# Kernel optimization log

Measured on AMD Instinct MI355X. Metric: run time of the kernel, lower is better.

## Reference

```python
import jax, jax.numpy as jnp
import numpy as np

B, C, H, W = 4, 256, 64, 64
CQ = C // 4


def setup_inputs() -> dict:
    key = jax.random.key(0)
    ks = jax.random.split(key, 16)
    s = 0.05
    return {
        "x1": jax.random.normal(ks[0], (B, C, H, W), jnp.float32),
        "x2": jax.random.normal(ks[1], (B, C, H, W), jnp.float32),
        "x3": jax.random.normal(ks[2], (B, C, H, W), jnp.float32),
        "xt": jax.random.normal(ks[3], (B, C, H, W), jnp.float32),
        "Wq": jax.random.normal(ks[4], (CQ, C), jnp.float32) * s,
        "bq": jax.random.normal(ks[5], (CQ,), jnp.float32) * s,
        "Wk": jax.random.normal(ks[6], (CQ, C), jnp.float32) * s,
        "bk": jax.random.normal(ks[7], (CQ,), jnp.float32) * s,
        "Wk2": jax.random.normal(ks[8], (CQ, C), jnp.float32) * s,
        "bk2": jax.random.normal(ks[9], (CQ,), jnp.float32) * s,
        "Wv": jax.random.normal(ks[10], (C, C), jnp.float32) * s,
        "bv": jax.random.normal(ks[11], (C,), jnp.float32) * s,
        "Wv2": jax.random.normal(ks[12], (C, C), jnp.float32) * s,
        "bv2": jax.random.normal(ks[13], (C,), jnp.float32) * s,
        "gamma": jax.random.normal(ks[14], (1,), jnp.float32) * 0.1,
        "gamma2": jax.random.normal(ks[15], (1,), jnp.float32) * 0.1,
    }


def _conv1x1(Wt, b, x):
    # 1x1 conv == per-pixel linear: (O, C) x (B, C, H, W) -> (B, O, H, W)
    return jnp.einsum('oc,bchw->bohw', Wt, x) + b[None, :, None, None]


def reference(x1, x2, x3, xt, Wq, bq, Wk, bk, Wk2, bk2, Wv, bv, Wv2, bv2, gamma, gamma2):
    b_, c_, h_, w_ = x1.shape
    n = h_ * w_
    q = _conv1x1(Wq, bq, x3).reshape(b_, -1, n)      # (B, C/4, N) queries
    k1 = _conv1x1(Wk, bk, x1).reshape(b_, -1, n)     # (B, C/4, N)
    k2 = _conv1x1(Wk2, bk2, x2).reshape(b_, -1, n)
    attn1 = jax.nn.softmax(jnp.einsum('bcn,bcm->bnm', q, k1), axis=-1)  # (B, N, N)
    attn2 = jax.nn.softmax(jnp.einsum('bcn,bcm->bnm', q, k2), axis=-1)
    attn = jax.nn.softmax(attn1 + attn2, axis=-1)    # re-softmax of summed attentions
    v = _conv1x1(Wv, bv, x3).reshape(b_, c_, n)
    out1 = jnp.einsum('bcm,bnm->bcn', v, attn).reshape(b_, c_, h_, w_)
    vt = _conv1x1(Wv2, bv2, xt).reshape(b_, c_, n)
    out2 = jnp.einsum('bcm,bnm->bcn', vt, attn).reshape(b_, c_, h_, w_)
    out = gamma[0] * out1 + x3
    out2 = gamma2[0] * out2 + xt
    return (attn, out, out2)
```

## Files before the change

### kernel.cpp

```cpp
#include <hip/hip_runtime.h>

#define Bn 4
#define Cn 256
#define CQn 64
#define Nn 4096

using f32x4  = __attribute__((ext_vector_type(4))) float;
using half4  = __attribute__((ext_vector_type(4))) _Float16;
using half8  = __attribute__((ext_vector_type(8))) _Float16;

#define MFMA_F16(a, b, c)  __builtin_amdgcn_mfma_f32_16x16x32_f16((a), (b), (c), 0, 0, 0)
#define SWZ(row, byte) ((unsigned)(byte) ^ ((((unsigned)(row)) & 7u) << 4))

__device__ __forceinline__ half8 lds_read8(const _Float16* base, int row, int slot) {
  return *(const half8*)((const char*)base + row * 128 + SWZ(row, slot * 16));
}
__device__ __forceinline__ void lds_write8(_Float16* base, int row, int slot, half8 v) {
  *(half8*)((char*)base + row * 128 + SWZ(row, slot * 16)) = v;
}

__global__ __launch_bounds__(256) void proj_all(
    const float* __restrict__ x1, const float* __restrict__ x2,
    const float* __restrict__ x3, const float* __restrict__ xt,
    const float* __restrict__ Wq, const float* __restrict__ bq,
    const float* __restrict__ Wk, const float* __restrict__ bk,
    const float* __restrict__ Wk2, const float* __restrict__ bk2,
    const float* __restrict__ Wv, const float* __restrict__ bv,
    const float* __restrict__ Wv2, const float* __restrict__ bv2,
    _Float16* __restrict__ qt, _Float16* __restrict__ k1t, _Float16* __restrict__ k2t,
    _Float16* __restrict__ v, _Float16* __restrict__ vt)
{
  const int p = blockIdx.z;
  const float* x    = (p == 0 || p == 3) ? x3 : (p == 1) ? x1 : (p == 2) ? x2 : xt;
  const float* W    = (p == 0) ? Wq : (p == 1) ? Wk : (p == 2) ? Wk2 : (p == 3) ? Wv : Wv2;
  const float* bias = (p == 0) ? bq : (p == 1) ? bk : (p == 2) ? bk2 : (p == 3) ? bv : bv2;

  const int b = blockIdx.y;
  const int n0 = blockIdx.x * 64;
  const int tid = threadIdx.x;
  const int w = tid >> 6, lane = tid & 63, quad = lane >> 4, l16 = lane & 15;

  __shared__ _Float16 xT[64 * 256];

  {
    const int nq = (tid & 15) * 4;
#pragma unroll
    for (int it = 0; it < 4; ++it) {
      const int cg = it * 64 + (tid >> 4) * 4;
      f32x4 xv[4];
#pragma unroll
      for (int ci = 0; ci < 4; ++ci)
        xv[ci] = *(const f32x4*)(x + ((size_t)b * Cn + cg + ci) * Nn + n0 + nq);
#pragma unroll
      for (int ni = 0; ni < 4; ++ni) {
        const int row = nq + ni;
        half4 hv;
#pragma unroll
        for (int ci = 0; ci < 4; ++ci) hv[ci] = (_Float16)xv[ci][ni];
        *(half4*)((char*)xT + row * 512 + SWZ(row, cg * 2)) = hv;
      }
    }
  }
  __syncthreads();

  if (p < 3) {
    _Float16* out = (p == 0) ? qt : (p == 1) ? k1t : k2t;
    const int row = w * 16 + l16;
    f32x4 acc[4] = {};
    for (int kst = 0; kst < 8; ++kst) {
      const half8 a = *(const half8*)((const char*)xT + row * 512 +
                                      SWZ(row, (kst * 4 + quad) * 16));
#pragma unroll
      for (int s = 0; s < 4; ++s) {
        const int o = s * 16 + l16;
        const f32x4 w0 = *(const f32x4*)(W + (size_t)o * Cn + kst * 32 + quad * 8);
        const f32x4 w1 = *(const f32x4*)(W + (size_t)o * Cn + kst * 32 + quad * 8 + 4);
        half8 bf;
#pragma unroll
        for (int j = 0; j < 4; ++j) { bf[j] = (_Float16)w0[j]; bf[4 + j] = (_Float16)w1[j]; }
        acc[s] = MFMA_F16(a, bf, acc[s]);
      }
    }
#pragma unroll
    for (int s = 0; s < 4; ++s) {
      const int o = s * 16 + l16;
      const float bb = bias[o];
#pragma unroll
      for (int r = 0; r < 4; ++r) {
        const int n = n0 + w * 16 + quad * 4 + r;
        out[((size_t)b * Nn + n) * CQn + o] = (_Float16)(acc[s][r] + bb);
      }
    }
  } else {
    _Float16* out = (p == 3) ? v : vt;
    f32x4 acc[4][4] = {};
    for (int kst = 0; kst < 8; ++kst) {
      half8 bt[4];
#pragma unroll
      for (int tt = 0; tt < 4; ++tt) {
        const int rowx = tt * 16 + l16;
        bt[tt] = *(const half8*)((const char*)xT + rowx * 512 +
                                 SWZ(rowx, (kst * 4 + quad) * 16));
      }
#pragma unroll
      for (int s = 0; s < 4; ++s) {
        const int o = w * 64 + s * 16 + l16;
        const f32x4 w0 = *(const f32x4*)(W + (size_t)o * Cn + kst * 32 + quad * 8);
        const f32x4 w1 = *(const f32x4*)(W + (size_t)o * Cn + kst * 32 + quad * 8 + 4);
        half8 a;
#pragma unroll
        for (int j = 0; j < 4; ++j) { a[j] = (_Float16)w0[j]; a[4 + j] = (_Float16)w1[j]; }
#pragma unroll
        for (int tt = 0; tt < 4; ++tt) acc[s][tt] = MFMA_F16(a, bt[tt], acc[s][tt]);
      }
    }
#pragma unroll
    for (int s = 0; s < 4; ++s) {
#pragma unroll
      for (int r = 0; r < 4; ++r) {
        const int o = w * 64 + s * 16 + quad * 4 + r;
        const float bb = bias[o];
#pragma unroll
        for (int tt = 0; tt < 4; ++tt) {
          const int n = n0 + tt * 16 + l16;
          out[((size_t)b * Cn + o) * Nn + n] = (_Float16)(acc[s][tt][r] + bb);
        }
      }
    }
  }
}

__global__ __launch_bounds__(1024, 4) void attn_flash(
    const _Float16* __restrict__ qt, const _Float16* __restrict__ k1t,
    const _Float16* __restrict__ k2t, const _Float16* __restrict__ v,
    const _Float16* __restrict__ vt,
    const float* __restrict__ x3, const float* __restrict__ xt,
    const float* __restrict__ gamma, const float* __restrict__ gamma2,
    float* __restrict__ attn, float* __restrict__ out1, float* __restrict__ out2)
{
  __shared__ _Float16 qT[64 * 64];
  __shared__ _Float16 Kt[2][2][64 * 64];
  __shared__ _Float16 Vt[2][256 * 64];
  __shared__ _Float16 ppT[64 * 64];
  __shared__ float red[16][2][16];
  __shared__ float rLs[64];

  const int i = blockIdx.x;
  const int b = (i & 7) >> 1;
  const int nt = ((i >> 3) << 1) | (i & 1);
  const int n0 = nt * 64;
  const int tid = threadIdx.x;
  const int w = tid >> 6, lane = tid & 63, quad = lane >> 4, l16 = lane & 15;
  const int ntw = w & 3;
  const int ms  = w >> 2;

  const _Float16* k1b = k1t + (size_t)b * Nn * CQn;
  const _Float16* k2b = k2t + (size_t)b * Nn * CQn;
  const _Float16* vb  = v   + (size_t)b * Cn * Nn;
  const _Float16* vtb = vt  + (size_t)b * Cn * Nn;
  const float g1 = gamma[0], g2 = gamma2[0];

  {
    const int row = tid >> 4, s8 = tid & 15;
    const half4 qv = *(const half4*)(qt + ((size_t)b * Nn + n0 + row) * CQn + s8 * 4);
    *(half4*)((char*)qT + row * 128 + SWZ(row, s8 * 8)) = qv;
  }

  const int k_te  = tid >> 9;
  const int k_row = (tid >> 3) & 63;
  const int k_sl  = tid & 7;
  const _Float16* kSrcBase = (k_te ? k2b : k1b) + (size_t)k_row * CQn + k_sl * 8;
  _Float16* kDst0 = (_Float16*)((char*)Kt[0][k_te] + k_row * 128 + SWZ(k_row, k_sl * 16));
  _Float16* kDst1 = (_Float16*)((char*)Kt[1][k_te] + k_row * 128 + SWZ(k_row, k_sl * 16));
  *(half8*)kDst0 = *(const half8*)kSrcBase;
  __syncthreads();

  const half8 aq0 = lds_read8(qT, ntw * 16 + l16, quad);
  const half8 aq1 = lds_read8(qT, ntw * 16 + l16, 4 + quad);
  const int krow = ms * 16 + l16;

  float l1a[4] = {0.f, 0.f, 0.f, 0.f}, l2a[4] = {0.f, 0.f, 0.f, 0.f};
#pragma unroll 1
  for (int t = 0; t < 64; ++t) {
    const int mn = ((t + 1) & 63) * 64;
    const half8 kreg = *(const half8*)(kSrcBase + (size_t)mn * CQn);
    const _Float16* Kc0 = Kt[t & 1][0];
    const _Float16* Kc1 = Kt[t & 1][1];
    const half8 kb0 = lds_read8(Kc0, krow, quad);
    const half8 kb1 = lds_read8(Kc0, krow, 4 + quad);
    const half8 kb2 = lds_read8(Kc1, krow, quad);
    const half8 kb3 = lds_read8(Kc1, krow, 4 + quad);
    f32x4 S1 = {}; S1 = MFMA_F16(aq0, kb0, S1); S1 = MFMA_F16(aq1, kb1, S1);
    f32x4 S2 = {}; S2 = MFMA_F16(aq0, kb2, S2); S2 = MFMA_F16(aq1, kb3, S2);
#pragma unroll
    for (int r = 0; r < 4; ++r) { l1a[r] += __expf(S1[r]); l2a[r] += __expf(S2[r]); }
    *(half8*)(((t + 1) & 1) ? kDst1 : kDst0) = kreg;
    __syncthreads();
  }
#pragma unroll
  for (int r = 0; r < 4; ++r)
#pragma unroll
    for (int off = 1; off < 16; off <<= 1) {
      l1a[r] += __shfl_xor(l1a[r], off);
      l2a[r] += __shfl_xor(l2a[r], off);
    }
  if (l16 == 0)
#pragma unroll
    for (int r = 0; r < 4; ++r) { red[w][0][quad * 4 + r] = l1a[r]; red[w][1][quad * 4 + r] = l2a[r]; }
  __syncthreads();
  float lg1[4], lg2[4];
#pragma unroll
  for (int r = 0; r < 4; ++r) {
    const int nn = quad * 4 + r;
    float s1 = 0.f, s2 = 0.f;
#pragma unroll
    for (int msk = 0; msk < 4; ++msk) { s1 += red[ntw + 4 * msk][0][nn]; s2 += red[ntw + 4 * msk][1][nn]; }
    lg1[r] = __logf(s1); lg2[r] = __logf(s2);
  }
  __syncthreads();

  float La[4] = {0.f, 0.f, 0.f, 0.f};
#pragma unroll 1
  for (int t = 0; t < 64; ++t) {
    const int mn = ((t + 1) & 63) * 64;
    const half8 kreg = *(const half8*)(kSrcBase + (size_t)mn * CQn);
    const _Float16* Kc0 = Kt[t & 1][0];
    const _Float16* Kc1 = Kt[t & 1][1];
    const half8 kb0 = lds_read8(Kc0, krow, quad);
    const half8 kb1 = lds_read8(Kc0, krow, 4 + quad);
    const half8 kb2 = lds_read8(Kc1, krow, quad);
    const half8 kb3 = lds_read8(Kc1, krow, 4 + quad);
    f32x4 S1 = {}; S1 = MFMA_F16(aq0, kb0, S1); S1 = MFMA_F16(aq1, kb1, S1);
    f32x4 S2 = {}; S2 = MFMA_F16(aq0, kb2, S2); S2 = MFMA_F16(aq1, kb3, S2);
#pragma unroll
    for (int r = 0; r < 4; ++r) {
      const float a1 = __expf(S1[r] - lg1[r]);
      const float a2 = __expf(S2[r] - lg2[r]);
      La[r] += __expf(a1 + a2);
    }
    *(half8*)(((t + 1) & 1) ? kDst1 : kDst0) = kreg;
    __syncthreads();
  }
#pragma unroll
  for (int r = 0; r < 4; ++r)
#pragma unroll
    for (int off = 1; off < 16; off <<= 1) La[r] += __shfl_xor(La[r], off);
  if (l16 == 0)
#pragma unroll
    for (int r = 0; r < 4; ++r) red[w][0][quad * 4 + r] = La[r];
  __syncthreads();
  if (tid < 64) {
    float s = 0.f;
#pragma unroll
    for (int msk = 0; msk < 4; ++msk) s += red[(tid >> 4) + 4 * msk][0][tid & 15];
    rLs[tid] = 1.0f / s;
  }
  __syncthreads();

  const int v_te = tid >> 9;
  const int v_c  = (tid >> 1) & 255;
  const int v_s0 = (tid & 1) * 4;
  const _Float16* vSrcBase = (v_te ? vtb : vb) + (size_t)v_c * Nn + v_s0 * 8;
  char* vDstB = (char*)Vt[v_te] + v_c * 128;

  f32x4 acc[4][2] = {};
#pragma unroll 1
  for (int t = 0; t < 64; ++t) {
    const int m0 = t * 64;
    const int mn = ((t + 1) & 63) * 64;
    half8 vreg[4];
#pragma unroll
    for (int j = 0; j < 4; ++j) vreg[j] = *(const half8*)(vSrcBase + m0 + j * 8);
    const half8 kreg = *(const half8*)(kSrcBase + (size_t)mn * CQn);
    const _Float16* Kc0 = Kt[t & 1][0];
    const _Float16* Kc1 = Kt[t & 1][1];
    const half8 kb0 = lds_read8(Kc0, krow, quad);
    const half8 kb1 = lds_read8(Kc0, krow, 4 + quad);
    const half8 kb2 = lds_read8(Kc1, krow, quad);
    const half8 kb3 = lds_read8(Kc1, krow, 4 + quad);
    f32x4 S1 = {}; S1 = MFMA_F16(aq0, kb0, S1); S1 = MFMA_F16(aq1, kb1, S1);
    f32x4 S2 = {}; S2 = MFMA_F16(aq0, kb2, S2); S2 = MFMA_F16(aq1, kb3, S2);
#pragma unroll
    for (int r = 0; r < 4; ++r) {
      const float a1 = __expf(S1[r] - lg1[r]);
      const float a2 = __expf(S2[r] - lg2[r]);
      const float ppv = __expf(a1 + a2);
      const int prow = ntw * 16 + quad * 4 + r;
      const int pcol = ms * 16 + l16;
      *(_Float16*)((char*)ppT + prow * 128 + SWZ(prow, pcol * 2)) = (_Float16)ppv;
    }
#pragma unroll
    for (int j = 0; j < 4; ++j)
      *(half8*)(vDstB + SWZ(v_c, (v_s0 + j) * 16)) = vreg[j];
    *(half8*)(((t + 1) & 1) ? kDst1 : kDst0) = kreg;
    __syncthreads();
#pragma unroll
    for (int kk = 0; kk < 2; ++kk) {
      const half8 A1 = lds_read8(Vt[0], w * 16 + l16, kk * 4 + quad);
      const half8 A2 = lds_read8(Vt[1], w * 16 + l16, kk * 4 + quad);
#pragma unroll
      for (int nn = 0; nn < 4; ++nn) {
        const half8 pb = lds_read8(ppT, nn * 16 + l16, kk * 4 + quad);
        acc[nn][0] = MFMA_F16(A1, pb, acc[nn][0]);
        acc[nn][1] = MFMA_F16(A2, pb, acc[nn][1]);
      }
    }
    {
      const int row = tid >> 4, c4 = (tid & 15) * 4;
      const half4 h = *(const half4*)((const char*)ppT + row * 128 + SWZ(row, c4 * 2));
      const float rl = rLs[row];
      f32x4 o;
#pragma unroll
      for (int jj = 0; jj < 4; ++jj) o[jj] = (float)h[jj] * rl;
      *(f32x4*)(attn + ((size_t)b * Nn + n0 + row) * Nn + m0 + c4) = o;
    }
    __syncthreads();
  }

#pragma unroll
  for (int nn = 0; nn < 4; ++nn) {
    const float rl = rLs[nn * 16 + l16];
#pragma unroll
    for (int r = 0; r < 4; ++r) {
      const int c = w * 16 + quad * 4 + r;
      const size_t base = ((size_t)b * Cn + c) * Nn + n0 + nn * 16 + l16;
      out1[base] = g1 * acc[nn][0][r] * rl + x3[base];
      out2[base] = g2 * acc[nn][1][r] * rl + xt[base];
    }
  }
}

extern "C" void kernel_launch(void* const* d_in, const int* in_sizes, int n_in,
                              void* d_out, int out_size, void* d_ws, size_t ws_size,
                              hipStream_t stream) {
  const float* x1  = (const float*)d_in[0];
  const float* x2  = (const float*)d_in[1];
  const float* x3  = (const float*)d_in[2];
  const float* xt  = (const float*)d_in[3];
  const float* Wq  = (const float*)d_in[4];
  const float* bq  = (const float*)d_in[5];
  const float* Wk  = (const float*)d_in[6];
  const float* bk  = (const float*)d_in[7];
  const float* Wk2 = (const float*)d_in[8];
  const float* bk2 = (const float*)d_in[9];
  const float* Wv  = (const float*)d_in[10];
  const float* bv  = (const float*)d_in[11];
  const float* Wv2 = (const float*)d_in[12];
  const float* bv2 = (const float*)d_in[13];
  const float* gamma  = (const float*)d_in[14];
  const float* gamma2 = (const float*)d_in[15];

  float* outp = (float*)d_out;
  float* attn = outp;
  float* out1 = outp + (size_t)Bn * Nn * Nn;
  float* out2 = out1 + (size_t)Bn * Cn * Nn;

  _Float16* qt  = (_Float16*)d_ws;
  _Float16* k1t = qt + (size_t)Bn * Nn * CQn;
  _Float16* k2t = k1t + (size_t)Bn * Nn * CQn;
  _Float16* v   = k2t + (size_t)Bn * Nn * CQn;
  _Float16* vt  = v + (size_t)Bn * Cn * Nn;

  proj_all<<<dim3(Nn / 64, Bn, 5), 256, 0, stream>>>(
      x1, x2, x3, xt, Wq, bq, Wk, bk, Wk2, bk2, Wv, bv, Wv2, bv2,
      qt, k1t, k2t, v, vt);
  attn_flash<<<dim3(Bn * Nn / 64), 1024, 0, stream>>>(
      qt, k1t, k2t, v, vt, x3, xt, gamma, gamma2, attn, out1, out2);
}
```

Baseline: 607.5 us.

## Load Q/K/V fragments directly from global and triple-buffer P tile in LDS

Drops LDS staging for Q, K and V. Each wave now reads its MFMA operand fragments straight from global memory, relying on cache reuse across waves. The PV loop uses a three-slot P buffer and computes the next tile's P before the single barrier, which removes one __syncthreads per iteration and the per-iteration K/V LDS writes. In exchange it adds redundant global and L2 traffic, because every wave fetches its own K and V fragments.

```diff
diff --git a/kernel.cpp b/kernel.cpp
--- a/kernel.cpp
+++ b/kernel.cpp
@@ -14,9 +14,6 @@
 
 __device__ __forceinline__ half8 lds_read8(const _Float16* base, int row, int slot) {
   return *(const half8*)((const char*)base + row * 128 + SWZ(row, slot * 16));
-}
-__device__ __forceinline__ void lds_write8(_Float16* base, int row, int slot, half8 v) {
-  *(half8*)((char*)base + row * 128 + SWZ(row, slot * 16)) = v;
 }
 
 __global__ __launch_bounds__(256) void proj_all(
@@ -138,10 +135,7 @@
     const float* __restrict__ gamma, const float* __restrict__ gamma2,
     float* __restrict__ attn, float* __restrict__ out1, float* __restrict__ out2)
 {
-  __shared__ _Float16 qT[64 * 64];
-  __shared__ _Float16 Kt[2][2][64 * 64];
-  __shared__ _Float16 Vt[2][256 * 64];
-  __shared__ _Float16 ppT[64 * 64];
+  __shared__ _Float16 ppT[3][64 * 64];
   __shared__ float red[16][2][16];
   __shared__ float rLs[64];
 
@@ -160,42 +154,27 @@
   const _Float16* vtb = vt  + (size_t)b * Cn * Nn;
   const float g1 = gamma[0], g2 = gamma2[0];
 
-  {
-    const int row = tid >> 4, s8 = tid & 15;
-    const half4 qv = *(const half4*)(qt + ((size_t)b * Nn + n0 + row) * CQn + s8 * 4);
-    *(half4*)((char*)qT + row * 128 + SWZ(row, s8 * 8)) = qv;
-  }
-
-  const int k_te  = tid >> 9;
-  const int k_row = (tid >> 3) & 63;
-  const int k_sl  = tid & 7;
-  const _Float16* kSrcBase = (k_te ? k2b : k1b) + (size_t)k_row * CQn + k_sl * 8;
-  _Float16* kDst0 = (_Float16*)((char*)Kt[0][k_te] + k_row * 128 + SWZ(k_row, k_sl * 16));
-  _Float16* kDst1 = (_Float16*)((char*)Kt[1][k_te] + k_row * 128 + SWZ(k_row, k_sl * 16));
-  *(half8*)kDst0 = *(const half8*)kSrcBase;
-  __syncthreads();
-
-  const half8 aq0 = lds_read8(qT, ntw * 16 + l16, quad);
-  const half8 aq1 = lds_read8(qT, ntw * 16 + l16, 4 + quad);
-  const int krow = ms * 16 + l16;
+  const _Float16* qrow = qt + ((size_t)b * Nn + n0 + ntw * 16 + l16) * CQn;
+  const half8 aq0 = *(const half8*)(qrow + quad * 8);
+  const half8 aq1 = *(const half8*)(qrow + 32 + quad * 8);
+
+  const size_t kstep = (size_t)64 * CQn;
+  const _Float16* k1r0 = k1b + (size_t)(ms * 16 + l16) * CQn + quad * 8;
+  const _Float16* k2r0 = k2b + (size_t)(ms * 16 + l16) * CQn + quad * 8;
 
   float l1a[4] = {0.f, 0.f, 0.f, 0.f}, l2a[4] = {0.f, 0.f, 0.f, 0.f};
-#pragma unroll 1
+#pragma unroll 2
   for (int t = 0; t < 64; ++t) {
-    const int mn = ((t + 1) & 63) * 64;
-    const half8 kreg = *(const half8*)(kSrcBase + (size_t)mn * CQn);
-    const _Float16* Kc0 = Kt[t & 1][0];
-    const _Float16* Kc1 = Kt[t & 1][1];
-    const half8 kb0 = lds_read8(Kc0, krow, quad);
-    const half8 kb1 = lds_read8(Kc0, krow, 4 + quad);
-    const half8 kb2 = lds_read8(Kc1, krow, quad);
-    const half8 kb3 = lds_read8(Kc1, krow, 4 + quad);
+    const _Float16* k1r = k1r0 + (size_t)t * kstep;
+    const _Float16* k2r = k2r0 + (size_t)t * kstep;
+    const half8 kb0 = *(const half8*)(k1r);
+    const half8 kb1 = *(const half8*)(k1r + 32);
+    const half8 kb2 = *(const half8*)(k2r);
+    const half8 kb3 = *(const half8*)(k2r + 32);
     f32x4 S1 = {}; S1 = MFMA_F16(aq0, kb0, S1); S1 = MFMA_F16(aq1, kb1, S1);
     f32x4 S2 = {}; S2 = MFMA_F16(aq0, kb2, S2); S2 = MFMA_F16(aq1, kb3, S2);
 #pragma unroll
     for (int r = 0; r < 4; ++r) { l1a[r] += __expf(S1[r]); l2a[r] += __expf(S2[r]); }
-    *(half8*)(((t + 1) & 1) ? kDst1 : kDst0) = kreg;
-    __syncthreads();
   }
 #pragma unroll
   for (int r = 0; r < 4; ++r)
@@ -220,16 +199,14 @@
   __syncthreads();
 
   float La[4] = {0.f, 0.f, 0.f, 0.f};
-#pragma unroll 1
+#pragma unroll 2
   for (int t = 0; t < 64; ++t) {
-    const int mn = ((t + 1) & 63) * 64;
-    const half8 kreg = *(const half8*)(kSrcBase + (size_t)mn * CQn);
-    const _Float16* Kc0 = Kt[t & 1][0];
-    const _Float16* Kc1 = Kt[t & 1][1];
-    const half8 kb0 = lds_read8(Kc0, krow, quad);
-    const half8 kb1 = lds_read8(Kc0, krow, 4 + quad);
-    const half8 kb2 = lds_read8(Kc1, krow, quad);
-    const half8 kb3 = lds_read8(Kc1, krow, 4 + quad);
+    const _Float16* k1r = k1r0 + (size_t)t * kstep;
+    const _Float16* k2r = k2r0 + (size_t)t * kstep;
+    const half8 kb0 = *(const half8*)(k1r);
+    const half8 kb1 = *(const half8*)(k1r + 32);
+    const half8 kb2 = *(const half8*)(k2r);
+    const half8 kb3 = *(const half8*)(k2r + 32);
     f32x4 S1 = {}; S1 = MFMA_F16(aq0, kb0, S1); S1 = MFMA_F16(aq1, kb1, S1);
     f32x4 S2 = {}; S2 = MFMA_F16(aq0, kb2, S2); S2 = MFMA_F16(aq1, kb3, S2);
 #pragma unroll
@@ -238,8 +215,6 @@
       const float a2 = __expf(S2[r] - lg2[r]);
       La[r] += __expf(a1 + a2);
     }
-    *(half8*)(((t + 1) & 1) ? kDst1 : kDst0) = kreg;
-    __syncthreads();
   }
 #pragma unroll
   for (int r = 0; r < 4; ++r)
@@ -257,27 +232,11 @@
   }
   __syncthreads();
 
-  const int v_te = tid >> 9;
-  const int v_c  = (tid >> 1) & 255;
-  const int v_s0 = (tid & 1) * 4;
-  const _Float16* vSrcBase = (v_te ? vtb : vb) + (size_t)v_c * Nn + v_s0 * 8;
-  char* vDstB = (char*)Vt[v_te] + v_c * 128;
-
-  f32x4 acc[4][2] = {};
-#pragma unroll 1
-  for (int t = 0; t < 64; ++t) {
-    const int m0 = t * 64;
-    const int mn = ((t + 1) & 63) * 64;
-    half8 vreg[4];
-#pragma unroll
-    for (int j = 0; j < 4; ++j) vreg[j] = *(const half8*)(vSrcBase + m0 + j * 8);
-    const half8 kreg = *(const half8*)(kSrcBase + (size_t)mn * CQn);
-    const _Float16* Kc0 = Kt[t & 1][0];
-    const _Float16* Kc1 = Kt[t & 1][1];
-    const half8 kb0 = lds_read8(Kc0, krow, quad);
-    const half8 kb1 = lds_read8(Kc0, krow, 4 + quad);
-    const half8 kb2 = lds_read8(Kc1, krow, quad);
-    const half8 kb3 = lds_read8(Kc1, krow, 4 + quad);
+  {
+    const half8 kb0 = *(const half8*)(k1r0);
+    const half8 kb1 = *(const half8*)(k1r0 + 32);
+    const half8 kb2 = *(const half8*)(k2r0);
+    const half8 kb3 = *(const half8*)(k2r0 + 32);
     f32x4 S1 = {}; S1 = MFMA_F16(aq0, kb0, S1); S1 = MFMA_F16(aq1, kb1, S1);
     f32x4 S2 = {}; S2 = MFMA_F16(aq0, kb2, S2); S2 = MFMA_F16(aq1, kb3, S2);
 #pragma unroll
@@ -287,34 +246,67 @@
       const float ppv = __expf(a1 + a2);
       const int prow = ntw * 16 + quad * 4 + r;
       const int pcol = ms * 16 + l16;
-      *(_Float16*)((char*)ppT + prow * 128 + SWZ(prow, pcol * 2)) = (_Float16)ppv;
-    }
-#pragma unroll
-    for (int j = 0; j < 4; ++j)
-      *(half8*)(vDstB + SWZ(v_c, (v_s0 + j) * 16)) = vreg[j];
-    *(half8*)(((t + 1) & 1) ? kDst1 : kDst0) = kreg;
+      *(_Float16*)((char*)ppT[0] + prow * 128 + SWZ(prow, pcol * 2)) = (_Float16)ppv;
+    }
+  }
+  __syncthreads();
+
+  const _Float16* v1r = vb  + (size_t)(w * 16 + l16) * Nn;
+  const _Float16* v2r = vtb + (size_t)(w * 16 + l16) * Nn;
+  const int arow = tid >> 4;
+  const int ac4  = (tid & 15) * 4;
+  const float arl = rLs[arow];
+  float* const abase = attn + ((size_t)b * Nn + n0 + arow) * Nn;
+
+  f32x4 acc[4][2] = {};
+#pragma unroll 1
+  for (int t = 0; t < 64; ++t) {
+    const int m0 = t * 64;
+    half8 va[2], vc[2];
+#pragma unroll
+    for (int kk = 0; kk < 2; ++kk) {
+      va[kk] = *(const half8*)(v1r + m0 + (kk * 4 + quad) * 8);
+      vc[kk] = *(const half8*)(v2r + m0 + (kk * 4 + quad) * 8);
+    }
+    {
+      const int tn = (t + 1) & 63;
+      const _Float16* k1r = k1r0 + (size_t)tn * kstep;
+      const _Float16* k2r = k2r0 + (size_t)tn * kstep;
+      const half8 kb0 = *(const half8*)(k1r);
+      const half8 kb1 = *(const half8*)(k1r + 32);
+      const half8 kb2 = *(const half8*)(k2r);
+      const half8 kb3 = *(const half8*)(k2r + 32);
+      f32x4 S1 = {}; S1 = MFMA_F16(aq0, kb0, S1); S1 = MFMA_F16(aq1, kb1, S1);
+      f32x4 S2 = {}; S2 = MFMA_F16(aq0, kb2, S2); S2 = MFMA_F16(aq1, kb3, S2);
+      _Float16* pN = ppT[(t + 1) % 3];
+#pragma unroll
+      for (int r = 0; r < 4; ++r) {
+        const float a1 = __expf(S1[r] - lg1[r]);
+        const float a2 = __expf(S2[r] - lg2[r]);
+        const float ppv = __expf(a1 + a2);
+        const int prow = ntw * 16 + quad * 4 + r;
+        const int pcol = ms * 16 + l16;
+        *(_Float16*)((char*)pN + prow * 128 + SWZ(prow, pcol * 2)) = (_Float16)ppv;
+      }
+    }
     __syncthreads();
+    const _Float16* pT = ppT[t % 3];
 #pragma unroll
     for (int kk = 0; kk < 2; ++kk) {
-      const half8 A1 = lds_read8(Vt[0], w * 16 + l16, kk * 4 + quad);
-      const half8 A2 = lds_read8(Vt[1], w * 16 + l16, kk * 4 + quad);
 #pragma unroll
       for (int nn = 0; nn < 4; ++nn) {
-        const half8 pb = lds_read8(ppT, nn * 16 + l16, kk * 4 + quad);
-        acc[nn][0] = MFMA_F16(A1, pb, acc[nn][0]);
-        acc[nn][1] = MFMA_F16(A2, pb, acc[nn][1]);
+        const half8 pb = lds_read8(pT, nn * 16 + l16, kk * 4 + quad);
+        acc[nn][0] = MFMA_F16(va[kk], pb, acc[nn][0]);
+        acc[nn][1] = MFMA_F16(vc[kk], pb, acc[nn][1]);
       }
     }
     {
-      const int row = tid >> 4, c4 = (tid & 15) * 4;
-      const half4 h = *(const half4*)((const char*)ppT + row * 128 + SWZ(row, c4 * 2));
-      const float rl = rLs[row];
+      const half4 h = *(const half4*)((const char*)pT + arow * 128 + SWZ(arow, ac4 * 2));
       f32x4 o;
 #pragma unroll
-      for (int jj = 0; jj < 4; ++jj) o[jj] = (float)h[jj] * rl;
-      *(f32x4*)(attn + ((size_t)b * Nn + n0 + row) * Nn + m0 + c4) = o;
-    }
-    __syncthreads();
+      for (int jj = 0; jj < 4; ++jj) o[jj] = (float)h[jj] * arl;
+      *(f32x4*)(abase + m0 + ac4) = o;
+    }
   }
 
 #pragma unroll
```

Measured after the change: 891.9 us. 46.8% more time.

## Load V operands straight to registers and software-pipeline P computation in PV loop

Applied to the files above, without the earlier changes.

The third pass no longer stages V/Vt tiles through LDS. Each wave loads its V fragments directly from global memory into registers as MFMA B operands and prefetches the next tile. P is double-buffered in LDS so the next tile's QK scores and exponentials are computed while the current tile's PV MFMAs run, which cuts one barrier per iteration. The output tiling is swapped so the epilogue does vectorized f32x4 stores, and Q is loaded straight to registers. The trade-off is more register pressure and uncoalesced 16-byte global reads of V spread across rows.

```diff
diff --git a/kernel.cpp b/kernel.cpp
--- a/kernel.cpp
+++ b/kernel.cpp
@@ -14,9 +14,6 @@
 
 __device__ __forceinline__ half8 lds_read8(const _Float16* base, int row, int slot) {
   return *(const half8*)((const char*)base + row * 128 + SWZ(row, slot * 16));
-}
-__device__ __forceinline__ void lds_write8(_Float16* base, int row, int slot, half8 v) {
-  *(half8*)((char*)base + row * 128 + SWZ(row, slot * 16)) = v;
 }
 
 __global__ __launch_bounds__(256) void proj_all(
@@ -138,10 +135,8 @@
     const float* __restrict__ gamma, const float* __restrict__ gamma2,
     float* __restrict__ attn, float* __restrict__ out1, float* __restrict__ out2)
 {
-  __shared__ _Float16 qT[64 * 64];
   __shared__ _Float16 Kt[2][2][64 * 64];
-  __shared__ _Float16 Vt[2][256 * 64];
-  __shared__ _Float16 ppT[64 * 64];
+  __shared__ _Float16 ppT[2][64 * 64];
   __shared__ float red[16][2][16];
   __shared__ float rLs[64];
 
@@ -160,30 +155,26 @@
   const _Float16* vtb = vt  + (size_t)b * Cn * Nn;
   const float g1 = gamma[0], g2 = gamma2[0];
 
-  {
-    const int row = tid >> 4, s8 = tid & 15;
-    const half4 qv = *(const half4*)(qt + ((size_t)b * Nn + n0 + row) * CQn + s8 * 4);
-    *(half4*)((char*)qT + row * 128 + SWZ(row, s8 * 8)) = qv;
-  }
+  const _Float16* qrow = qt + ((size_t)b * Nn + n0 + ntw * 16 + l16) * CQn;
+  const half8 aq0 = *(const half8*)(qrow + quad * 8);
+  const half8 aq1 = *(const half8*)(qrow + 32 + quad * 8);
 
   const int k_te  = tid >> 9;
   const int k_row = (tid >> 3) & 63;
   const int k_sl  = tid & 7;
+  const size_t kstep = (size_t)64 * CQn;
   const _Float16* kSrcBase = (k_te ? k2b : k1b) + (size_t)k_row * CQn + k_sl * 8;
   _Float16* kDst0 = (_Float16*)((char*)Kt[0][k_te] + k_row * 128 + SWZ(k_row, k_sl * 16));
   _Float16* kDst1 = (_Float16*)((char*)Kt[1][k_te] + k_row * 128 + SWZ(k_row, k_sl * 16));
   *(half8*)kDst0 = *(const half8*)kSrcBase;
   __syncthreads();
 
-  const half8 aq0 = lds_read8(qT, ntw * 16 + l16, quad);
-  const half8 aq1 = lds_read8(qT, ntw * 16 + l16, 4 + quad);
   const int krow = ms * 16 + l16;
 
   float l1a[4] = {0.f, 0.f, 0.f, 0.f}, l2a[4] = {0.f, 0.f, 0.f, 0.f};
 #pragma unroll 1
   for (int t = 0; t < 64; ++t) {
-    const int mn = ((t + 1) & 63) * 64;
-    const half8 kreg = *(const half8*)(kSrcBase + (size_t)mn * CQn);
+    const half8 kreg = *(const half8*)(kSrcBase + (size_t)((t + 1) & 63) * kstep);
     const _Float16* Kc0 = Kt[t & 1][0];
     const _Float16* Kc1 = Kt[t & 1][1];
     const half8 kb0 = lds_read8(Kc0, krow, quad);
@@ -222,8 +213,7 @@
   float La[4] = {0.f, 0.f, 0.f, 0.f};
 #pragma unroll 1
   for (int t = 0; t < 64; ++t) {
-    const int mn = ((t + 1) & 63) * 64;
-    const half8 kreg = *(const half8*)(kSrcBase + (size_t)mn * CQn);
+    const half8 kreg = *(const half8*)(kSrcBase + (size_t)((t + 1) & 63) * kstep);
     const _Float16* Kc0 = Kt[t & 1][0];
     const _Float16* Kc1 = Kt[t & 1][1];
     const half8 kb0 = lds_read8(Kc0, krow, quad);
@@ -241,6 +231,7 @@
     *(half8*)(((t + 1) & 1) ? kDst1 : kDst0) = kreg;
     __syncthreads();
   }
+  *(half8*)kDst1 = *(const half8*)(kSrcBase + kstep);
 #pragma unroll
   for (int r = 0; r < 4; ++r)
 #pragma unroll
@@ -257,23 +248,9 @@
   }
   __syncthreads();
 
-  const int v_te = tid >> 9;
-  const int v_c  = (tid >> 1) & 255;
-  const int v_s0 = (tid & 1) * 4;
-  const _Float16* vSrcBase = (v_te ? vtb : vb) + (size_t)v_c * Nn + v_s0 * 8;
-  char* vDstB = (char*)Vt[v_te] + v_c * 128;
-
-  f32x4 acc[4][2] = {};
-#pragma unroll 1
-  for (int t = 0; t < 64; ++t) {
-    const int m0 = t * 64;
-    const int mn = ((t + 1) & 63) * 64;
-    half8 vreg[4];
-#pragma unroll
-    for (int j = 0; j < 4; ++j) vreg[j] = *(const half8*)(vSrcBase + m0 + j * 8);
-    const half8 kreg = *(const half8*)(kSrcBase + (size_t)mn * CQn);
-    const _Float16* Kc0 = Kt[t & 1][0];
-    const _Float16* Kc1 = Kt[t & 1][1];
+  {
+    const _Float16* Kc0 = Kt[0][0];
+    const _Float16* Kc1 = Kt[0][1];
     const half8 kb0 = lds_read8(Kc0, krow, quad);
     const half8 kb1 = lds_read8(Kc0, krow, 4 + quad);
     const half8 kb2 = lds_read8(Kc1, krow, quad);
@@ -287,45 +264,115 @@
       const float ppv = __expf(a1 + a2);
       const int prow = ntw * 16 + quad * 4 + r;
       const int pcol = ms * 16 + l16;
-      *(_Float16*)((char*)ppT + prow * 128 + SWZ(prow, pcol * 2)) = (_Float16)ppv;
-    }
-#pragma unroll
-    for (int j = 0; j < 4; ++j)
-      *(half8*)(vDstB + SWZ(v_c, (v_s0 + j) * 16)) = vreg[j];
-    *(half8*)(((t + 1) & 1) ? kDst1 : kDst0) = kreg;
+      *(_Float16*)((char*)ppT[0] + prow * 128 + SWZ(prow, pcol * 2)) = (_Float16)ppv;
+    }
+  }
+  __syncthreads();
+
+  const int ni = w & 1, ci = w >> 1;
+  const _Float16* vA0 = vb  + (size_t)(ci * 32 +      l16) * Nn + quad * 8;
+  const _Float16* vA1 = vb  + (size_t)(ci * 32 + 16 + l16) * Nn + quad * 8;
+  const _Float16* vB0 = vtb + (size_t)(ci * 32 +      l16) * Nn + quad * 8;
+  const _Float16* vB1 = vtb + (size_t)(ci * 32 + 16 + l16) * Nn + quad * 8;
+
+  const int arow = tid >> 4;
+  const int ac4  = (tid & 15) * 4;
+  const float arl = rLs[arow];
+  float* const abase = attn + ((size_t)b * Nn + n0 + arow) * Nn;
+
+  half8 vcur[2][2][2];
+#pragma unroll
+  for (int kk = 0; kk < 2; ++kk) {
+    vcur[0][0][kk] = *(const half8*)(vA0 + kk * 32);
+    vcur[0][1][kk] = *(const half8*)(vA1 + kk * 32);
+    vcur[1][0][kk] = *(const half8*)(vB0 + kk * 32);
+    vcur[1][1][kk] = *(const half8*)(vB1 + kk * 32);
+  }
+
+  f32x4 acc[2][2][2] = {};
+#pragma unroll 1
+  for (int t = 0; t < 64; ++t) {
+    const int m0 = t * 64;
+    const _Float16* pTc = ppT[t & 1];
+#pragma unroll
+    for (int ns = 0; ns < 2; ++ns) {
+      const int prow = ni * 32 + ns * 16 + l16;
+#pragma unroll
+      for (int kk = 0; kk < 2; ++kk) {
+        const half8 ap = lds_read8(pTc, prow, kk * 4 + quad);
+#pragma unroll
+        for (int cs = 0; cs < 2; ++cs) {
+          acc[ns][cs][0] = MFMA_F16(ap, vcur[0][cs][kk], acc[ns][cs][0]);
+          acc[ns][cs][1] = MFMA_F16(ap, vcur[1][cs][kk], acc[ns][cs][1]);
+        }
+      }
+    }
+    {
+      const half4 h = *(const half4*)((const char*)pTc + arow * 128 + SWZ(arow, ac4 * 2));
+      f32x4 o;
+#pragma unroll
+      for (int jj = 0; jj < 4; ++jj) o[jj] = (float)h[jj] * arl;
+      *(f32x4*)(abase + m0 + ac4) = o;
+    }
+    const int mN = ((t + 1) & 63) * 64;
+    half8 vnx[2][2][2];
+#pragma unroll
+    for (int kk = 0; kk < 2; ++kk) {
+      vnx[0][0][kk] = *(const half8*)(vA0 + mN + kk * 32);
+      vnx[0][1][kk] = *(const half8*)(vA1 + mN + kk * 32);
+      vnx[1][0][kk] = *(const half8*)(vB0 + mN + kk * 32);
+      vnx[1][1][kk] = *(const half8*)(vB1 + mN + kk * 32);
+    }
+    const half8 kreg = *(const half8*)(kSrcBase + (size_t)((t + 2) & 63) * kstep);
+    {
+      const _Float16* Kc0 = Kt[(t + 1) & 1][0];
+      const _Float16* Kc1 = Kt[(t + 1) & 1][1];
+      const half8 kb0 = lds_read8(Kc0, krow, quad);
+      const half8 kb1 = lds_read8(Kc0, krow, 4 + quad);
+      const half8 kb2 = lds_read8(Kc1, krow, quad);
+      const half8 kb3 = lds_read8(Kc1, krow, 4 + quad);
+      f32x4 S1 = {}; S1 = MFMA_F16(aq0, kb0, S1); S1 = MFMA_F16(aq1, kb1, S1);
+      f32x4 S2 = {}; S2 = MFMA_F16(aq0, kb2, S2); S2 = MFMA_F16(aq1, kb3, S2);
+      _Float16* pN = ppT[(t + 1) & 1];
+#pragma unroll
+      for (int r = 0; r < 4; ++r) {
+        const float a1 = __expf(S1[r] - lg1[r]);
+        const float a2 = __expf(S2[r] - lg2[r]);
+        const float ppv = __expf(a1 + a2);
+        const int prow = ntw * 16 + quad * 4 + r;
+        const int pcol = ms * 16 + l16;
+        *(_Float16*)((char*)pN + prow * 128 + SWZ(prow, pcol * 2)) = (_Float16)ppv;
+      }
+    }
+    *(half8*)((t & 1) ? kDst1 : kDst0) = kreg;
     __syncthreads();
 #pragma unroll
-    for (int kk = 0; kk < 2; ++kk) {
-      const half8 A1 = lds_read8(Vt[0], w * 16 + l16, kk * 4 + quad);
-      const half8 A2 = lds_read8(Vt[1], w * 16 + l16, kk * 4 + quad);
-#pragma unroll
-      for (int nn = 0; nn < 4; ++nn) {
-        const half8 pb = lds_read8(ppT, nn * 16 + l16, kk * 4 + quad);
-        acc[nn][0] = MFMA_F16(A1, pb, acc[nn][0]);
-        acc[nn][1] = MFMA_F16(A2, pb, acc[nn][1]);
-      }
-    }
-    {
-      const int row = tid >> 4, c4 = (tid & 15) * 4;
-      const half4 h = *(const half4*)((const char*)ppT + row * 128 + SWZ(row, c4 * 2));
-      const float rl = rLs[row];
-      f32x4 o;
-#pragma unroll
-      for (int jj = 0; jj < 4; ++jj) o[jj] = (float)h[jj] * rl;
-      *(f32x4*)(attn + ((size_t)b * Nn + n0 + row) * Nn + m0 + c4) = o;
-    }
-    __syncthreads();
-  }
-
-#pragma unroll
-  for (int nn = 0; nn < 4; ++nn) {
-    const float rl = rLs[nn * 16 + l16];
-#pragma unroll
-    for (int r = 0; r < 4; ++r) {
-      const int c = w * 16 + quad * 4 + r;
-      const size_t base = ((size_t)b * Cn + c) * Nn + n0 + nn * 16 + l16;
-      out1[base] = g1 * acc[nn][0][r] * rl + x3[base];
-      out2[base] = g2 * acc[nn][1][r] * rl + xt[base];
+    for (int te = 0; te < 2; ++te)
+#pragma unroll
+      for (int cs = 0; cs < 2; ++cs)
+#pragma unroll
+        for (int kk = 0; kk < 2; ++kk) vcur[te][cs][kk] = vnx[te][cs][kk];
+  }
+
+#pragma unroll
+  for (int ns = 0; ns < 2; ++ns) {
+    f32x4 rv;
+#pragma unroll
+    for (int jj = 0; jj < 4; ++jj) rv[jj] = rLs[ni * 32 + ns * 16 + quad * 4 + jj];
+#pragma unroll
+    for (int cs = 0; cs < 2; ++cs) {
+      const int c = ci * 32 + cs * 16 + l16;
+      const size_t base = ((size_t)b * Cn + c) * Nn + n0 + ni * 32 + ns * 16 + quad * 4;
+      const f32x4 xr1 = *(const f32x4*)(x3 + base);
+      const f32x4 xr2 = *(const f32x4*)(xt + base);
+      f32x4 o1, o2;
+#pragma unroll
+      for (int jj = 0; jj < 4; ++jj) {
+        o1[jj] = g1 * acc[ns][cs][0][jj] * rv[jj] + xr1[jj];
+        o2[jj] = g2 * acc[ns][cs][1][jj] * rv[jj] + xr2[jj];
+      }
+      *(f32x4*)(out1 + base) = o1;
+      *(f32x4*)(out2 + base) = o2;
     }
   }
 }
```

After: 770.1 us. 1.27x slower.
